# Performance work log

Measured on AMD Instinct MI355X. Metric: run time of the kernel, lower is better.

The kernel has to match this reference:

```python
import jax, jax.numpy as jnp
import numpy as np

B, L, D, H = 4, 2048, 1024, 16
DH = D // H
SCALE = 1.0 / float(np.sqrt(DH))


def setup_inputs() -> dict:
    key = jax.random.key(0)
    ks = jax.random.split(key, 11)
    s = 0.02
    return {
        "q": jax.random.normal(ks[0], (B, L, D), jnp.float32),
        "k": jax.random.normal(ks[1], (B, L, D), jnp.float32),
        "v": jax.random.normal(ks[2], (B, L, D), jnp.float32),
        "Wq": jax.random.normal(ks[3], (D, D), jnp.float32) * s,
        "bq": jnp.zeros((D,), jnp.float32),
        "Wk": jax.random.normal(ks[4], (D, D), jnp.float32) * s,
        "bk": jnp.zeros((D,), jnp.float32),
        "Wv": jax.random.normal(ks[5], (D, D), jnp.float32) * s,
        "bv": jnp.zeros((D,), jnp.float32),
        "Wo": jax.random.normal(ks[6], (D, D), jnp.float32) * s,
        "bo": jnp.zeros((D,), jnp.float32),
    }


def _split_heads(x):
    # (B, L, D) -> (B, H, L, DH)
    b, l, _ = x.shape
    return x.reshape(b, l, H, DH).transpose(0, 2, 1, 3)


def reference(q, k, v, Wq, bq, Wk, bk, Wv, bv, Wo, bo):
    # torch Linear: y = x @ W.T + b
    qh = _split_heads(q @ Wq.T + bq)
    kh = _split_heads(k @ Wk.T + bk)
    vh = _split_heads(v @ Wv.T + bv)
    # Blocked loop in original == full attention: every q block sees all K/V.
    scores = jnp.einsum("bhqd,bhkd->bhqk", qh, kh) * SCALE
    attn = jax.nn.softmax(scores, axis=-1)  # dropout=0 (eval) -> identity
    out = jnp.einsum("bhqk,bhkd->bhqd", attn, vh)
    out = out.transpose(0, 2, 1, 3).reshape(q.shape[0], q.shape[1], D)
    return out @ Wo.T + bo
```

## Files before the change

kernel.cpp:

```cpp
#include <hip/hip_runtime.h>
#include <hip/hip_bf16.h>
#include <stdint.h>

#define NB  4
#define SEQ 2048
#define DIM 1024
#define NH  16
#define DHD 64
#define LOG2E 1.44269504088896340736f

typedef short short8 __attribute__((ext_vector_type(8)));
typedef float f32x4  __attribute__((ext_vector_type(4)));

__device__ __forceinline__ unsigned short f2bf(float f) {
  union { float f; uint32_t u; } x; x.f = f;
  uint32_t u = x.u;
  uint32_t r = (u + 0x7fffu + ((u >> 16) & 1u)) >> 16;
  return (unsigned short)r;
}

__device__ __forceinline__ uint32_t cvt_pk_bf16(float lo, float hi) {
  uint32_t r;
  asm("v_cvt_pk_bf16_f32 %0, %1, %2" : "=v"(r) : "v"(lo), "v"(hi));
  return r;
}

__device__ __forceinline__ void gload16(const void* g, void* l) {
  __builtin_amdgcn_global_load_lds(
      (const __attribute__((address_space(1))) uint32_t*)g,
      (__attribute__((address_space(3))) uint32_t*)l, 16, 0, 0);
}

__global__ void cvt_f32_bf16(const float* __restrict__ in,
                             unsigned short* __restrict__ out, int n4) {
  int i = blockIdx.x * blockDim.x + threadIdx.x;
  int stride = gridDim.x * blockDim.x;
  for (int j = i; j < n4; j += stride) {
    float4 v = reinterpret_cast<const float4*>(in)[j];
    ushort4 o;
    o.x = f2bf(v.x); o.y = f2bf(v.y); o.z = f2bf(v.z); o.w = f2bf(v.w);
    reinterpret_cast<ushort4*>(out)[j] = o;
  }
}

template <int MODE>
__global__ __launch_bounds__(256, 2) void gemm_bt(
    const unsigned short* __restrict__ A,
    const unsigned short* __restrict__ Bm,
    const float* __restrict__ bias,
    float* __restrict__ Cf,
    unsigned short* __restrict__ Cb,
    int M, int N, int K, float scale) {
  __shared__ uint4 smem[4096];

  const int tid  = threadIdx.x;
  const int lane = tid & 63;
  const int wid  = tid >> 6;
  const int cpx  = gridDim.x >> 3;
  const int wg   = (blockIdx.x & 7) * cpx + (blockIdx.x >> 3);
  const int nbn  = N >> 7;
  const int bm   = wg / nbn;
  const int bn   = wg % nbn;
  const int wrow = (wid >> 1) * 64;
  const int wcol = (wid & 1) * 64;

  f32x4 acc[4][4] = {};

  const unsigned short* pa[4];
  const unsigned short* pb[4];
  uint4* la[4];
  uint4* lb[4];
#pragma unroll
  for (int i = 0; i < 4; ++i) {
    int c   = tid + (i << 8);
    int row = c >> 3;
    int kc  = (c & 7) ^ (row & 7);
    pa[i] = A  + (size_t)(bm * 128 + row) * K + kc * 8;
    pb[i] = Bm + (size_t)(bn * 128 + row) * K + kc * 8;
    la[i] = smem + c;
    lb[i] = smem + 2048 + c;
  }
  auto stage = [&](int kt, int buf) {
#pragma unroll
    for (int i = 0; i < 4; ++i) {
      gload16(pa[i] + kt * 64, la[i] + buf * 1024);
      gload16(pb[i] + kt * 64, lb[i] + buf * 1024);
    }
  };

  stage(0, 0);
  __syncthreads();

  const int NT = K >> 6;
  for (int kt = 0; kt < NT; ++kt) {
    const int cur = kt & 1;
    if (kt + 1 < NT) stage(kt + 1, cur ^ 1);

#pragma unroll
    for (int s = 0; s < 2; ++s) {
      short8 af[4], bfr[4];
#pragma unroll
      for (int mt = 0; mt < 4; ++mt) {
        int row = wrow + mt * 16 + (lane & 15);
        int ch  = ((s << 2) + (lane >> 4)) ^ (row & 7);
        af[mt]  = __builtin_bit_cast(short8, smem[cur * 1024 + row * 8 + ch]);
      }
#pragma unroll
      for (int nt = 0; nt < 4; ++nt) {
        int row = wcol + nt * 16 + (lane & 15);
        int ch  = ((s << 2) + (lane >> 4)) ^ (row & 7);
        bfr[nt] = __builtin_bit_cast(short8, smem[2048 + cur * 1024 + row * 8 + ch]);
      }
      __builtin_amdgcn_s_setprio(1);
#pragma unroll
      for (int mt = 0; mt < 4; ++mt)
#pragma unroll
        for (int nt = 0; nt < 4; ++nt)
          acc[mt][nt] = __builtin_amdgcn_mfma_f32_16x16x32_bf16(af[mt], bfr[nt], acc[mt][nt], 0, 0, 0);
      __builtin_amdgcn_s_setprio(0);
    }
    __syncthreads();
  }

  if (MODE == 0) {
    float* cf = (float*)smem;
#pragma unroll
    for (int nt = 0; nt < 4; ++nt) {
      int tcol = wcol + nt * 16 + (lane & 15);
      float bv = bias[bn * 128 + tcol];
#pragma unroll
      for (int mt = 0; mt < 4; ++mt)
#pragma unroll
        for (int r = 0; r < 4; ++r) {
          int trow = wrow + mt * 16 + (lane >> 4) * 4 + r;
          cf[trow * 128 + tcol] = acc[mt][nt][r] + bv;
        }
    }
    __syncthreads();
#pragma unroll
    for (int it = 0; it < 16; ++it) {
      int idx = tid + it * 256;
      int row = idx >> 5, seg = idx & 31;
      uint4 val = ((uint4*)cf)[idx];
      *reinterpret_cast<uint4*>(Cf + (size_t)(bm * 128 + row) * N + bn * 128 + seg * 4) = val;
    }
  } else if (MODE == 1) {
    unsigned short* cb = (unsigned short*)smem;
#pragma unroll
    for (int nt = 0; nt < 4; ++nt) {
      int tcol = wcol + nt * 16 + (lane & 15);
      float bv = bias[bn * 128 + tcol];
#pragma unroll
      for (int mt = 0; mt < 4; ++mt)
#pragma unroll
        for (int r = 0; r < 4; ++r) {
          int trow = wrow + mt * 16 + (lane >> 4) * 4 + r;
          cb[trow * 128 + tcol] = f2bf((acc[mt][nt][r] + bv) * scale);
        }
    }
    __syncthreads();
#pragma unroll
    for (int it = 0; it < 8; ++it) {
      int idx = tid + it * 256;
      int row = idx >> 4, seg = idx & 15;
      uint4 val = ((uint4*)cb)[idx];
      int gcol = bn * 128 + seg * 8;
      int h = gcol >> 6, dh = gcol & 63;
      int grow = bm * 128 + row;
      int b = grow >> 11, lq = grow & 2047;
      *reinterpret_cast<uint4*>(Cb + ((size_t)((b << 4) + h) * SEQ + lq) * DHD + dh) = val;
    }
  } else {
    unsigned short* cb = (unsigned short*)smem;
#pragma unroll
    for (int nt = 0; nt < 4; ++nt) {
      int tcol = wcol + nt * 16 + (lane & 15);
      float bv = bias[bn * 128 + tcol];
#pragma unroll
      for (int mt = 0; mt < 4; ++mt) {
        int trow0 = wrow + mt * 16 + (lane >> 4) * 4;
        uint2 pk;
        pk.x = cvt_pk_bf16((acc[mt][nt][0] + bv) * scale, (acc[mt][nt][1] + bv) * scale);
        pk.y = cvt_pk_bf16((acc[mt][nt][2] + bv) * scale, (acc[mt][nt][3] + bv) * scale);
        *reinterpret_cast<uint2*>(cb + tcol * 128 + trow0) = pk;
      }
    }
    __syncthreads();
#pragma unroll
    for (int it = 0; it < 8; ++it) {
      int idx = tid + it * 256;
      int col = idx >> 4, seg = idx & 15;
      uint4 val = ((uint4*)cb)[idx];
      int gcol = bn * 128 + col;
      int h = gcol >> 6, dh = gcol & 63;
      int grow = bm * 128 + seg * 8;
      int b = grow >> 11, lq = grow & 2047;
      *reinterpret_cast<uint4*>(Cb + ((size_t)((b << 4) + h) * DHD + dh) * SEQ + lq) = val;
    }
  }
}

__global__ __launch_bounds__(256, 4) void attn_kernel(
    const unsigned short* __restrict__ Qh,
    const unsigned short* __restrict__ Kh,
    const unsigned short* __restrict__ Vt,
    unsigned short* __restrict__ O) {
  __shared__ uint4 Kls[2][64 * 8];
  __shared__ uint4 Vls[2][64 * 8];
  __shared__ uint4 Pls[4][16 * 8];

  const int tid  = threadIdx.x;
  const int lane = tid & 63;
  const int wid  = tid >> 6;
  const int wg   = (blockIdx.x & 7) * 256 + (blockIdx.x >> 3);
  const int bh   = wg >> 5;
  const int qt   = wg & 31;
  const int qloc = lane & 15;
  const int grp  = lane >> 4;

  const unsigned short* Qb = Qh + (size_t)bh * SEQ * DHD;
  const unsigned short* Kb = Kh + (size_t)bh * SEQ * DHD;
  const unsigned short* Vb = Vt + (size_t)bh * DHD * SEQ;

  const unsigned short* pk[2];
  const unsigned short* pv[2];
  uint4* lk[2];
  uint4* lv[2];
#pragma unroll
  for (int i = 0; i < 2; ++i) {
    int c   = tid + (i << 8);
    int row = c >> 3;
    int kc  = (c & 7) ^ (row & 7);
    pk[i] = Kb + (size_t)row * DHD + kc * 8;
    pv[i] = Vb + (size_t)row * SEQ + kc * 8;
    lk[i] = &Kls[0][c];
    lv[i] = &Vls[0][c];
  }
  auto stage = [&](int kt, int buf) {
#pragma unroll
    for (int i = 0; i < 2; ++i) {
      gload16(pk[i] + (size_t)kt * 64 * DHD, lk[i] + buf * 512);
      gload16(pv[i] + kt * 64,               lv[i] + buf * 512);
    }
  };

  stage(0, 0);

  const int qrow = qt * 64 + wid * 16 + qloc;
  short8 qf[2];
#pragma unroll
  for (int s = 0; s < 2; ++s)
    qf[s] = *reinterpret_cast<const short8*>(Qb + (size_t)qrow * DHD + s * 32 + grp * 8);

  const short8 ones = {0x3F80, 0x3F80, 0x3F80, 0x3F80, 0x3F80, 0x3F80, 0x3F80, 0x3F80};

  __syncthreads();

  float logbias = 0.f;
  f32x4 lsum = {0.f, 0.f, 0.f, 0.f};
  f32x4 acc_o[4] = {};

  const int NT = SEQ / 64;
  for (int kt = 0; kt < NT; ++kt) {
    const int cur = kt & 1;
    if (kt + 1 < NT) stage(kt + 1, cur ^ 1);

    f32x4 sc[4];
    __builtin_amdgcn_s_setprio(1);
#pragma unroll
    for (int j = 0; j < 4; ++j) {
      f32x4 a = {logbias, logbias, logbias, logbias};
#pragma unroll
      for (int s = 0; s < 2; ++s) {
        int krow  = j * 16 + qloc;
        int ch    = ((s << 2) + grp) ^ (krow & 7);
        short8 kf = __builtin_bit_cast(short8, Kls[cur][krow * 8 + ch]);
        a = __builtin_amdgcn_mfma_f32_16x16x32_bf16(kf, qf[s], a, 0, 0, 0);
      }
      sc[j] = a;
    }
    __builtin_amdgcn_s_setprio(0);

#pragma unroll
    for (int j = 0; j < 4; ++j)
#pragma unroll
      for (int r = 0; r < 4; ++r) sc[j][r] = exp2f(sc[j][r]);

    char* pwb = (char*)&Pls[wid][0];
#pragma unroll
    for (int j = 0; j < 4; ++j)
#pragma unroll
      for (int h = 0; h < 2; ++h) {
        uint32_t d32 = cvt_pk_bf16(sc[j][2 * h], sc[j][2 * h + 1]);
        int key2 = (j * 16 + grp * 4 + 2 * h) * 2;
        int byte = qloc * 128 + ((((key2 >> 4)) ^ (qloc & 7)) << 4) + (key2 & 15);
        *(uint32_t*)(pwb + byte) = d32;
      }

    short8 pf[2];
#pragma unroll
    for (int s = 0; s < 2; ++s) {
      int ch = ((s << 2) + grp) ^ (qloc & 7);
      pf[s] = __builtin_bit_cast(short8, Pls[wid][qloc * 8 + ch]);
    }
    __builtin_amdgcn_s_setprio(1);
#pragma unroll
    for (int nt = 0; nt < 4; ++nt) {
#pragma unroll
      for (int s = 0; s < 2; ++s) {
        int vrow  = nt * 16 + qloc;
        int ch    = ((s << 2) + grp) ^ (vrow & 7);
        short8 vf = __builtin_bit_cast(short8, Vls[cur][vrow * 8 + ch]);
        acc_o[nt] = __builtin_amdgcn_mfma_f32_16x16x32_bf16(vf, pf[s], acc_o[nt], 0, 0, 0);
      }
    }
#pragma unroll
    for (int s = 0; s < 2; ++s)
      lsum = __builtin_amdgcn_mfma_f32_16x16x32_bf16(ones, pf[s], lsum, 0, 0, 0);
    __builtin_amdgcn_s_setprio(0);

    if (__any(lsum[0] > 7.9e28f)) {
      const float ds = 5.421010862e-20f;
      logbias -= 64.f;
#pragma unroll
      for (int nt = 0; nt < 4; ++nt)
#pragma unroll
        for (int r = 0; r < 4; ++r) acc_o[nt][r] *= ds;
#pragma unroll
      for (int r = 0; r < 4; ++r) lsum[r] *= ds;
    }

    __syncthreads();
  }

  const float inv = 1.0f / lsum[0];
  char* pwb = (char*)&Pls[wid][0];
#pragma unroll
  for (int nt = 0; nt < 4; ++nt)
#pragma unroll
    for (int h = 0; h < 2; ++h) {
      uint32_t d32 = cvt_pk_bf16(acc_o[nt][2 * h] * inv, acc_o[nt][2 * h + 1] * inv);
      int d2   = (nt * 16 + grp * 4 + 2 * h) * 2;
      int byte = qloc * 128 + ((((d2 >> 4)) ^ (qloc & 7)) << 4) + (d2 & 15);
      *(uint32_t*)(pwb + byte) = d32;
    }
  const int b = bh >> 4, h = bh & 15;
#pragma unroll
  for (int pass = 0; pass < 2; ++pass) {
    int row = pass * 8 + (lane >> 3);
    int ch  = (lane & 7) ^ (row & 7);
    uint4 val = Pls[wid][row * 8 + ch];
    int rowg  = qt * 64 + wid * 16 + row;
    *reinterpret_cast<uint4*>(O + ((size_t)(b * SEQ + rowg)) * DIM + (h << 6) + ((lane & 7) << 3)) = val;
  }
}

extern "C" void kernel_launch(void* const* d_in, const int* in_sizes, int n_in,
                              void* d_out, int out_size, void* d_ws, size_t ws_size,
                              hipStream_t stream) {
  (void)in_sizes; (void)n_in; (void)out_size; (void)ws_size;
  const float* q  = (const float*)d_in[0];
  const float* k  = (const float*)d_in[1];
  const float* v  = (const float*)d_in[2];
  const float* Wq = (const float*)d_in[3];
  const float* bq = (const float*)d_in[4];
  const float* Wk = (const float*)d_in[5];
  const float* bk = (const float*)d_in[6];
  const float* Wv = (const float*)d_in[7];
  const float* bv = (const float*)d_in[8];
  const float* Wo = (const float*)d_in[9];
  const float* bo = (const float*)d_in[10];
  float* out = (float*)d_out;

  char* ws = (char*)d_ws;
  const size_t MB = 1024 * 1024;
  unsigned short* X   = (unsigned short*)(ws + 0);
  unsigned short* WX  = (unsigned short*)(ws + 16 * MB);
  unsigned short* Qhp = (unsigned short*)(ws + 18 * MB);
  unsigned short* Khp = (unsigned short*)(ws + 34 * MB);
  unsigned short* Vtp = (unsigned short*)(ws + 50 * MB);

  const int nTok = NB * SEQ * DIM;
  const int nW   = DIM * DIM;
  const int M    = NB * SEQ;
  dim3 gg((M / 128) * (DIM / 128));

  cvt_f32_bf16<<<2048, 256, 0, stream>>>(q, X, nTok / 4);
  cvt_f32_bf16<<<1024, 256, 0, stream>>>(Wq, WX, nW / 4);
  gemm_bt<1><<<gg, 256, 0, stream>>>(X, WX, bq, nullptr, Qhp, M, DIM, DIM, 0.125f * LOG2E);
  cvt_f32_bf16<<<2048, 256, 0, stream>>>(k, X, nTok / 4);
  cvt_f32_bf16<<<1024, 256, 0, stream>>>(Wk, WX, nW / 4);
  gemm_bt<1><<<gg, 256, 0, stream>>>(X, WX, bk, nullptr, Khp, M, DIM, DIM, 1.0f);
  cvt_f32_bf16<<<2048, 256, 0, stream>>>(v, X, nTok / 4);
  cvt_f32_bf16<<<1024, 256, 0, stream>>>(Wv, WX, nW / 4);
  gemm_bt<2><<<gg, 256, 0, stream>>>(X, WX, bv, nullptr, Vtp, M, DIM, DIM, 1.0f);
  attn_kernel<<<NB * NH * (SEQ / 64), 256, 0, stream>>>(Qhp, Khp, Vtp, X);
  cvt_f32_bf16<<<1024, 256, 0, stream>>>(Wo, WX, nW / 4);
  gemm_bt<0><<<gg, 256, 0, stream>>>(X, WX, bo, out, nullptr, M, DIM, DIM, 1.0f);
}
```

Baseline: 247.6 us.

## Process 32 query rows per wave to reuse K/V fragments across two query blocks

The attention kernel now handles 128 query rows per workgroup (32 per wave), so each K and V fragment read from LDS feeds two MFMA query blocks instead of one. This halves the number of workgroups and the total K/V global-to-LDS traffic. The P buffer uses a padded 144-byte row stride in place of the XOR swizzle, and the logbias is added before exp2 rather than seeded into the accumulator. The trade is higher register pressure, reflected in launch bounds lowered from 4 to 3 waves per SIMD, and fewer blocks in the grid.

```diff
diff --git a/kernel.cpp b/kernel.cpp
--- a/kernel.cpp
+++ b/kernel.cpp
@@ -200,23 +200,24 @@
   }
 }
 
-__global__ __launch_bounds__(256, 4) void attn_kernel(
+__global__ __launch_bounds__(256, 3) void attn_kernel(
     const unsigned short* __restrict__ Qh,
     const unsigned short* __restrict__ Kh,
     const unsigned short* __restrict__ Vt,
     unsigned short* __restrict__ O) {
-  __shared__ uint4 Kls[2][64 * 8];
-  __shared__ uint4 Vls[2][64 * 8];
-  __shared__ uint4 Pls[4][16 * 8];
+  __shared__ uint4 Kls[2][512];
+  __shared__ uint4 Vls[2][512];
+  __shared__ uint4 Pls[4][32 * 9];
 
   const int tid  = threadIdx.x;
   const int lane = tid & 63;
   const int wid  = tid >> 6;
-  const int wg   = (blockIdx.x & 7) * 256 + (blockIdx.x >> 3);
-  const int bh   = wg >> 5;
-  const int qt   = wg & 31;
+  const int wg   = (blockIdx.x & 7) * 128 + (blockIdx.x >> 3);
+  const int bh   = wg >> 4;
+  const int qt   = wg & 15;
   const int qloc = lane & 15;
   const int grp  = lane >> 4;
+  const int q7   = qloc & 7;
 
   const unsigned short* Qb = Qh + (size_t)bh * SEQ * DHD;
   const unsigned short* Kb = Kh + (size_t)bh * SEQ * DHD;
@@ -246,112 +247,133 @@
 
   stage(0, 0);
 
-  const int qrow = qt * 64 + wid * 16 + qloc;
-  short8 qf[2];
-#pragma unroll
-  for (int s = 0; s < 2; ++s)
-    qf[s] = *reinterpret_cast<const short8*>(Qb + (size_t)qrow * DHD + s * 32 + grp * 8);
+  short8 qf[2][2];
+#pragma unroll
+  for (int qb = 0; qb < 2; ++qb) {
+    int qrow = qt * 128 + wid * 32 + qb * 16 + qloc;
+#pragma unroll
+    for (int s = 0; s < 2; ++s)
+      qf[qb][s] = *reinterpret_cast<const short8*>(Qb + (size_t)qrow * DHD + s * 32 + grp * 8);
+  }
 
   const short8 ones = {0x3F80, 0x3F80, 0x3F80, 0x3F80, 0x3F80, 0x3F80, 0x3F80, 0x3F80};
+  char* pwb = (char*)&Pls[wid][0];
 
   __syncthreads();
 
   float logbias = 0.f;
-  f32x4 lsum = {0.f, 0.f, 0.f, 0.f};
-  f32x4 acc_o[4] = {};
+  f32x4 lsum[2] = {};
+  f32x4 acc_o[4][2] = {};
 
   const int NT = SEQ / 64;
   for (int kt = 0; kt < NT; ++kt) {
     const int cur = kt & 1;
     if (kt + 1 < NT) stage(kt + 1, cur ^ 1);
 
-    f32x4 sc[4];
+    f32x4 sc[4][2];
     __builtin_amdgcn_s_setprio(1);
 #pragma unroll
     for (int j = 0; j < 4; ++j) {
-      f32x4 a = {logbias, logbias, logbias, logbias};
+      short8 kf[2];
 #pragma unroll
       for (int s = 0; s < 2; ++s) {
-        int krow  = j * 16 + qloc;
-        int ch    = ((s << 2) + grp) ^ (krow & 7);
-        short8 kf = __builtin_bit_cast(short8, Kls[cur][krow * 8 + ch]);
-        a = __builtin_amdgcn_mfma_f32_16x16x32_bf16(kf, qf[s], a, 0, 0, 0);
-      }
-      sc[j] = a;
+        int krow = j * 16 + qloc;
+        int ch   = ((s << 2) + grp) ^ q7;
+        kf[s] = __builtin_bit_cast(short8, Kls[cur][krow * 8 + ch]);
+      }
+#pragma unroll
+      for (int qb = 0; qb < 2; ++qb) {
+        f32x4 a = {0.f, 0.f, 0.f, 0.f};
+        a = __builtin_amdgcn_mfma_f32_16x16x32_bf16(kf[0], qf[qb][0], a, 0, 0, 0);
+        a = __builtin_amdgcn_mfma_f32_16x16x32_bf16(kf[1], qf[qb][1], a, 0, 0, 0);
+        sc[j][qb] = a;
+      }
     }
     __builtin_amdgcn_s_setprio(0);
 
 #pragma unroll
     for (int j = 0; j < 4; ++j)
 #pragma unroll
-      for (int r = 0; r < 4; ++r) sc[j][r] = exp2f(sc[j][r]);
-
-    char* pwb = (char*)&Pls[wid][0];
-#pragma unroll
-    for (int j = 0; j < 4; ++j)
-#pragma unroll
-      for (int h = 0; h < 2; ++h) {
-        uint32_t d32 = cvt_pk_bf16(sc[j][2 * h], sc[j][2 * h + 1]);
-        int key2 = (j * 16 + grp * 4 + 2 * h) * 2;
-        int byte = qloc * 128 + ((((key2 >> 4)) ^ (qloc & 7)) << 4) + (key2 & 15);
-        *(uint32_t*)(pwb + byte) = d32;
-      }
-
-    short8 pf[2];
-#pragma unroll
-    for (int s = 0; s < 2; ++s) {
-      int ch = ((s << 2) + grp) ^ (qloc & 7);
-      pf[s] = __builtin_bit_cast(short8, Pls[wid][qloc * 8 + ch]);
-    }
+      for (int qb = 0; qb < 2; ++qb) {
+        float p0 = exp2f(sc[j][qb][0] + logbias);
+        float p1 = exp2f(sc[j][qb][1] + logbias);
+        float p2 = exp2f(sc[j][qb][2] + logbias);
+        float p3 = exp2f(sc[j][qb][3] + logbias);
+        uint2 w;
+        w.x = cvt_pk_bf16(p0, p1);
+        w.y = cvt_pk_bf16(p2, p3);
+        *(uint2*)(pwb + (qb * 16 + qloc) * 144 + j * 32 + grp * 8) = w;
+      }
+
+    short8 pf[2][2];
+#pragma unroll
+    for (int qb = 0; qb < 2; ++qb)
+#pragma unroll
+      for (int t = 0; t < 2; ++t)
+        pf[qb][t] = *(const short8*)(pwb + (qb * 16 + qloc) * 144 + t * 64 + grp * 16);
+
     __builtin_amdgcn_s_setprio(1);
 #pragma unroll
-    for (int nt = 0; nt < 4; ++nt) {
-#pragma unroll
-      for (int s = 0; s < 2; ++s) {
-        int vrow  = nt * 16 + qloc;
-        int ch    = ((s << 2) + grp) ^ (vrow & 7);
-        short8 vf = __builtin_bit_cast(short8, Vls[cur][vrow * 8 + ch]);
-        acc_o[nt] = __builtin_amdgcn_mfma_f32_16x16x32_bf16(vf, pf[s], acc_o[nt], 0, 0, 0);
-      }
-    }
-#pragma unroll
-    for (int s = 0; s < 2; ++s)
-      lsum = __builtin_amdgcn_mfma_f32_16x16x32_bf16(ones, pf[s], lsum, 0, 0, 0);
+    for (int db = 0; db < 4; ++db) {
+      short8 vf[2];
+#pragma unroll
+      for (int t = 0; t < 2; ++t) {
+        int vrow = db * 16 + qloc;
+        int ch   = ((t << 2) + grp) ^ q7;
+        vf[t] = __builtin_bit_cast(short8, Vls[cur][vrow * 8 + ch]);
+      }
+#pragma unroll
+      for (int qb = 0; qb < 2; ++qb) {
+        acc_o[db][qb] = __builtin_amdgcn_mfma_f32_16x16x32_bf16(vf[0], pf[qb][0], acc_o[db][qb], 0, 0, 0);
+        acc_o[db][qb] = __builtin_amdgcn_mfma_f32_16x16x32_bf16(vf[1], pf[qb][1], acc_o[db][qb], 0, 0, 0);
+      }
+    }
+#pragma unroll
+    for (int qb = 0; qb < 2; ++qb) {
+      lsum[qb] = __builtin_amdgcn_mfma_f32_16x16x32_bf16(ones, pf[qb][0], lsum[qb], 0, 0, 0);
+      lsum[qb] = __builtin_amdgcn_mfma_f32_16x16x32_bf16(ones, pf[qb][1], lsum[qb], 0, 0, 0);
+    }
     __builtin_amdgcn_s_setprio(0);
 
-    if (__any(lsum[0] > 7.9e28f)) {
+    if (__any(fmaxf(lsum[0][0], lsum[1][0]) > 7.9e28f)) {
       const float ds = 5.421010862e-20f;
       logbias -= 64.f;
 #pragma unroll
-      for (int nt = 0; nt < 4; ++nt)
-#pragma unroll
-        for (int r = 0; r < 4; ++r) acc_o[nt][r] *= ds;
-#pragma unroll
-      for (int r = 0; r < 4; ++r) lsum[r] *= ds;
+      for (int db = 0; db < 4; ++db)
+#pragma unroll
+        for (int qb = 0; qb < 2; ++qb)
+#pragma unroll
+          for (int r = 0; r < 4; ++r) acc_o[db][qb][r] *= ds;
+#pragma unroll
+      for (int qb = 0; qb < 2; ++qb)
+#pragma unroll
+        for (int r = 0; r < 4; ++r) lsum[qb][r] *= ds;
     }
 
     __syncthreads();
   }
 
-  const float inv = 1.0f / lsum[0];
-  char* pwb = (char*)&Pls[wid][0];
-#pragma unroll
-  for (int nt = 0; nt < 4; ++nt)
-#pragma unroll
-    for (int h = 0; h < 2; ++h) {
-      uint32_t d32 = cvt_pk_bf16(acc_o[nt][2 * h] * inv, acc_o[nt][2 * h + 1] * inv);
-      int d2   = (nt * 16 + grp * 4 + 2 * h) * 2;
-      int byte = qloc * 128 + ((((d2 >> 4)) ^ (qloc & 7)) << 4) + (d2 & 15);
-      *(uint32_t*)(pwb + byte) = d32;
+  const float inv0 = 1.0f / lsum[0][0];
+  const float inv1 = 1.0f / lsum[1][0];
+#pragma unroll
+  for (int db = 0; db < 4; ++db)
+#pragma unroll
+    for (int qb = 0; qb < 2; ++qb) {
+      float inv = qb ? inv1 : inv0;
+      uint2 w;
+      w.x = cvt_pk_bf16(acc_o[db][qb][0] * inv, acc_o[db][qb][1] * inv);
+      w.y = cvt_pk_bf16(acc_o[db][qb][2] * inv, acc_o[db][qb][3] * inv);
+      *(uint2*)(pwb + (qb * 16 + qloc) * 144 + db * 32 + grp * 8) = w;
     }
   const int b = bh >> 4, h = bh & 15;
 #pragma unroll
-  for (int pass = 0; pass < 2; ++pass) {
-    int row = pass * 8 + (lane >> 3);
-    int ch  = (lane & 7) ^ (row & 7);
-    uint4 val = Pls[wid][row * 8 + ch];
-    int rowg  = qt * 64 + wid * 16 + row;
-    *reinterpret_cast<uint4*>(O + ((size_t)(b * SEQ + rowg)) * DIM + (h << 6) + ((lane & 7) << 3)) = val;
+  for (int pass = 0; pass < 4; ++pass) {
+    int idx = pass * 64 + lane;
+    int row = idx >> 3;
+    int ck  = idx & 7;
+    uint4 val = *(const uint4*)(pwb + row * 144 + ck * 16);
+    int rowg = qt * 128 + wid * 32 + row;
+    *reinterpret_cast<uint4*>(O + ((size_t)(b * SEQ + rowg)) * DIM + (h << 6) + ck * 8) = val;
   }
 }
 
@@ -394,7 +416,7 @@
   cvt_f32_bf16<<<2048, 256, 0, stream>>>(v, X, nTok / 4);
   cvt_f32_bf16<<<1024, 256, 0, stream>>>(Wv, WX, nW / 4);
   gemm_bt<2><<<gg, 256, 0, stream>>>(X, WX, bv, nullptr, Vtp, M, DIM, DIM, 1.0f);
-  attn_kernel<<<NB * NH * (SEQ / 64), 256, 0, stream>>>(Qhp, Khp, Vtp, X);
+  attn_kernel<<<NB * NH * (SEQ / 128), 256, 0, stream>>>(Qhp, Khp, Vtp, X);
   cvt_f32_bf16<<<1024, 256, 0, stream>>>(Wo, WX, nW / 4);
   gemm_bt<0><<<gg, 256, 0, stream>>>(X, WX, bo, out, nullptr, M, DIM, DIM, 1.0f);
 }
```

New measurement: 246.1 us. No clear change (-0.6%).
